# Kernel tuning notes

Hardware: AMD Instinct MI355X
Metric: run time of the kernel (lower is better)

## Reference

```python
import jax, jax.numpy as jnp
import numpy as np

NUM_HEADS = 8

def _gelu(x):
    return jax.nn.gelu(x, approximate=False)

def _ln(x, w, b, eps=1e-5):
    m = x.mean(-1, keepdims=True)
    v = ((x - m) ** 2).mean(-1, keepdims=True)
    return (x - m) / jnp.sqrt(v + eps) * w + b

def _conv(x, w, pad):
    return jax.lax.conv_general_dilated(x, w, (1, 1), [(pad, pad), (pad, pad)],
                                        dimension_numbers=('NCHW', 'OIHW', 'NCHW'))

def _dwconv(x, w):
    return jax.lax.conv_general_dilated(x, w, (1, 1), [(1, 1), (1, 1)],
                                        feature_group_count=x.shape[1],
                                        dimension_numbers=('NCHW', 'OIHW', 'NCHW'))

def setup_inputs():
    B, T, N, C, K = 4, 3, 4096, 256, 100
    ks = jax.random.split(jax.random.key(0), 16)
    p = lambda i, shape: (0.02 * jax.random.normal(ks[i], shape)).astype(jnp.float32)
    z = lambda n: jnp.zeros((n,), jnp.float32)
    return {
        'x': jax.random.normal(ks[0], (B, N, C), jnp.float32),
        'mem': jax.random.normal(ks[1], (B * T, N, C), jnp.float32),
        'conv1_w': p(2, (C, C, 7, 7)), 'conv1_b': z(C),
        'conv2_w': p(3, (C, C, 1, 1)), 'conv2_b': z(C),
        'conv3_w': p(4, (K, C, 1, 1)),
        'sim_alpha': jnp.ones((1,), jnp.float32), 'sim_beta': jnp.zeros((1,), jnp.float32),
        'ln_w': jnp.ones((C,), jnp.float32), 'ln_b': z(C),
        'q_w': p(5, (C, C)), 'q_b': z(C),
        'k_w': p(6, (C, C)), 'k_b': z(C),
        'v_w': p(7, (C, C)), 'v_b': z(C),
        'proj_w': p(8, (C, C)), 'proj_b': z(C),
        'fc1_w': p(9, (4 * C, C)), 'fc1_b': z(4 * C),
        'dw_w': p(10, (4 * C, 1, 3, 3)), 'dw_b': z(4 * C),
        'fc2_w': p(11, (C, 4 * C)), 'fc2_b': z(C),
        'H': 64, 'W': 64, 't': 3,
    }

def reference(x, mem, conv1_w, conv1_b, conv2_w, conv2_b, conv3_w, sim_alpha, sim_beta,
              ln_w, ln_b, q_w, q_b, k_w, k_b, v_w, v_b, proj_w, proj_b,
              fc1_w, fc1_b, dw_w, dw_b, fc2_w, fc2_b, H, W, t):
    B, N, C = x.shape
    T = t + 1
    # stack memory frames with current frame: [B, T, N, C]
    xt = jnp.concatenate([mem.reshape(B, t, N, C), x[:, None]], axis=1)
    img = xt.reshape(B * T, N, C).transpose(0, 2, 1).reshape(B * T, C, H, W)
    h = _gelu(_conv(img, conv1_w, 3) + conv1_b[:, None, None])
    h = _gelu(_conv(h, conv2_w, 0) + conv2_b[:, None, None])
    cz = _conv(h, conv3_w, 0)                      # [B*T, K, H, W]
    K = cz.shape[1]
    center = jax.nn.softmax(cz.reshape(B, T, K, N), axis=-1)
    center = jnp.einsum('btkn,btnc->btkc', center, xt)  # cluster centers [B,T,K,C]
    last, prev = center[:, -1], center[:, :-1]
    num = jnp.einsum('bkc,bskc->bsk', last, prev)
    den = jnp.maximum(jnp.linalg.norm(last, axis=-1)[:, None] * jnp.linalg.norm(prev, axis=-1), 1e-8)
    cos = jax.nn.sigmoid(sim_beta + sim_alpha * (num / den))  # [B, T-1, K]
    C_in = last + (cos[..., None] * prev).sum(axis=1)
    C_in = _ln(C_in, ln_w, ln_b)
    # cross-attention: queries = current frame tokens, keys/values = centers
    hd = C // NUM_HEADS
    q = (x @ q_w.T + q_b).reshape(B, N, NUM_HEADS, hd) * (hd ** -0.5)
    k = (C_in @ k_w.T + k_b).reshape(B, K, NUM_HEADS, hd)
    v = (C_in @ v_w.T + v_b).reshape(B, K, NUM_HEADS, hd)
    attn = jax.nn.softmax(jnp.einsum('bnhd,bkhd->bhnk', q, k), axis=-1)
    o = jnp.einsum('bhnk,bkhd->bnhd', attn, v).reshape(B, N, C)
    o = o @ proj_w.T + proj_b
    out = x + _ln(o, ln_w, ln_b)
    # MLP with depthwise conv
    y = out @ fc1_w.T + fc1_b                      # [B, N, 4C]
    yi = y.transpose(0, 2, 1).reshape(B, 4 * C, H, W)
    yi = _dwconv(yi, dw_w) + dw_b[:, None, None]
    y = _gelu(yi.reshape(B, 4 * C, N).transpose(0, 2, 1))
    y = y @ fc2_w.T + fc2_b
    return out + _ln(y, ln_w, ln_b)
```

## Files before the change

kernel.cpp:

```cpp
#include <hip/hip_runtime.h>
#include <math.h>

#define NN 4096
#define CC 256
#define HH 64
#define BT 16
#define KCC 100
#define NHH 8
#define HDD 32
#define C4 1024

typedef unsigned short bf16_t;
typedef short s16x8 __attribute__((ext_vector_type(8)));
typedef float f32x4 __attribute__((ext_vector_type(4)));
typedef float f32x16 __attribute__((ext_vector_type(16)));

__device__ __forceinline__ float bf2f(bf16_t h) {
  return __uint_as_float(((unsigned)h) << 16);
}
__device__ __forceinline__ bf16_t f2bf(float f) {
  unsigned u = __float_as_uint(f);
  return (bf16_t)((u + 0x7FFFu + ((u >> 16) & 1u)) >> 16);
}

__device__ __forceinline__ float gelu_f(float x) {
  return 0.5f * x * (1.0f + erff(x * 0.7071067811865475f));
}

__device__ __forceinline__ void g2l16(const void* g, void* l) {
  __builtin_amdgcn_global_load_lds((const __attribute__((address_space(1))) void*)g,
                                   (__attribute__((address_space(3))) void*)l, 16, 0, 0);
}

__device__ __forceinline__ float block_sum256(float v) {
  __shared__ float sh[4];
#pragma unroll
  for (int off = 32; off; off >>= 1) v += __shfl_xor(v, off, 64);
  __syncthreads();
  if ((threadIdx.x & 63) == 0) sh[threadIdx.x >> 6] = v;
  __syncthreads();
  return sh[0] + sh[1] + sh[2] + sh[3];
}

__device__ __forceinline__ const float* xt_base(const float* x, const float* mem, int bt) {
  int b = bt >> 2, tt = bt & 3;
  return (tt < 3) ? (mem + (size_t)(b * 3 + tt) * NN * CC)
                  : (x + (size_t)b * NN * CC);
}

__global__ __launch_bounds__(256) void prologue(const float* __restrict__ x,
                                                const float* __restrict__ mem,
                                                bf16_t* __restrict__ xtb,
                                                const float* __restrict__ w1,
                                                bf16_t* __restrict__ wtb,
                                                const float* __restrict__ c2w,
                                                const float* __restrict__ c3w,
                                                const float* __restrict__ qw,
                                                const float* __restrict__ pw,
                                                const float* __restrict__ f1w,
                                                const float* __restrict__ f2w,
                                                bf16_t* __restrict__ wbz) {
  int bid = blockIdx.x;
  int tid = threadIdx.x;
  if (bid < 16384) {
    int i = bid * 256 + tid;
    int c4 = i & 63;
    int n = (i >> 6) & 4095;
    int bt = i >> 18;
    const float* src = xt_base(x, mem, bt) + (size_t)n * CC + c4 * 4;
    float4 v = *(const float4*)src;
    ushort4 o;
    o.x = f2bf(v.x); o.y = f2bf(v.y); o.z = f2bf(v.z); o.w = f2bf(v.w);
    *(ushort4*)(xtb + (size_t)i * 4) = o;
  } else if (bid < 19520) {
    int i = (bid - 16384) * 256 + tid;
    int cj = i & 7;
    int t = i >> 3;
    int co = t & 63; t >>= 6;
    int oc = t & 3; t >>= 2;
    int kx = t % 7; t /= 7;
    int cq = t & 3; t >>= 2;
    int cg = t & 7;
    int ky = t >> 3;
    int ci = cg * 32 + oc * 8 + cj;
    int cog = cq * 64 + co;
    wtb[i] = f2bf(w1[((size_t)(cog * CC + ci) * 7 + ky) * 7 + kx]);
  } else {
    int j = (bid - 19520) * 256 + tid;
    float v;
    if (j < 65536) v = c2w[j];
    else if (j < 91136) v = c3w[j - 65536];
    else if (j < 156672) v = qw[j - 91136];
    else if (j < 222208) v = pw[j - 156672];
    else if (j < 484352) v = f1w[j - 222208];
    else v = f2w[j - 484352];
    wbz[j] = f2bf(v);
  }
}

__global__ __launch_bounds__(1024, 4) void conv1_mfma(const bf16_t* __restrict__ xtb,
                                                      const bf16_t* __restrict__ wtb,
                                                      const float* __restrict__ bias,
                                                      bf16_t* __restrict__ h1) {
  int bid = blockIdx.x;
  int cq = bid & 3;
  int rem = bid >> 2;
  int bt = rem & 15;
  int rb = rem >> 4;
  int r0 = rb * 16;
  int co0 = cq * 64;
  int tid = threadIdx.x;
  int wv = tid >> 6;
  int lane = tid & 63;
  int l31 = lane & 31;
  int h = lane >> 5;
  __shared__ __align__(16) short As[22][4][70][8];
  __shared__ __align__(16) short Ws[2][7][4][64][8];
  {
    s16x8 z = {0, 0, 0, 0, 0, 0, 0, 0};
    for (int i = tid; i < 22 * 4 * 70; i += 1024) *(s16x8*)((short*)As + i * 8) = z;
  }
  __syncthreads();
  f32x16 acc[2][2] = {};
  const bf16_t* xb = xtb + (size_t)bt * (NN * CC);
  for (int cig = 0; cig < 8; ++cig) {
    int ci0 = cig * 32;
    for (int t = wv; t < 88; t += 16) {
      int rr = t >> 2, go = t & 3;
      int r = r0 - 3 + rr;
      if (r >= 0 && r < HH) {
        const bf16_t* gsrc = xb + ((size_t)(r * 64 + lane)) * CC + ci0 + go * 8;
        g2l16(gsrc, &As[rr][go][3][0]);
      }
    }
    {
      const bf16_t* wk = wtb + ((size_t)((0 * 8 + cig) * 4 + cq)) * (1792 * 8);
      for (int t = wv; t < 28; t += 16)
        g2l16(wk + (size_t)t * 512 + lane * 8, (short*)Ws[0] + t * 512);
    }
    __syncthreads();
    for (int ky = 0; ky < 7; ++ky) {
      int cur = ky & 1;
      if (ky < 6) {
        const bf16_t* wk = wtb + ((size_t)(((ky + 1) * 8 + cig) * 4 + cq)) * (1792 * 8);
        for (int t = wv; t < 28; t += 16)
          g2l16(wk + (size_t)t * 512 + lane * 8, (short*)Ws[cur ^ 1] + t * 512);
      }
#pragma unroll
      for (int kx = 0; kx < 7; ++kx) {
        s16x8 fa[2][2], fb[2][2];
#pragma unroll
        for (int mt = 0; mt < 2; ++mt)
#pragma unroll
          for (int ks = 0; ks < 2; ++ks) {
            fa[mt][ks] = *(const s16x8*)&As[wv + ky][ks * 2 + h][mt * 32 + l31 + kx][0];
            fb[mt][ks] = *(const s16x8*)&Ws[cur][kx][ks * 2 + h][mt * 32 + l31][0];
          }
#pragma unroll
        for (int ks = 0; ks < 2; ++ks)
#pragma unroll
          for (int mt = 0; mt < 2; ++mt)
#pragma unroll
            for (int nt = 0; nt < 2; ++nt)
              acc[mt][nt] = __builtin_amdgcn_mfma_f32_32x32x16_bf16(
                  fa[mt][ks], fb[nt][ks], acc[mt][nt], 0, 0, 0);
      }
      __syncthreads();
    }
  }
  int row = r0 + wv;
  const size_t xbase = (size_t)bt * (NN * CC);
#pragma unroll
  for (int nt = 0; nt < 2; ++nt) {
    int co = co0 + nt * 32 + l31;
    float bs = bias[co];
#pragma unroll
    for (int mt = 0; mt < 2; ++mt) {
#pragma unroll
      for (int rg = 0; rg < 16; ++rg) {
        int px = mt * 32 + (rg & 3) + 8 * (rg >> 2) + 4 * h;
        float vv = acc[mt][nt][rg] + bs;
        h1[xbase + (size_t)(row * 64 + px) * CC + co] = f2bf(gelu_f(vv));
      }
    }
  }
}

__global__ __launch_bounds__(512) void conv23(const bf16_t* __restrict__ bh1,
                                              const bf16_t* __restrict__ w2,
                                              const float* __restrict__ b2,
                                              const bf16_t* __restrict__ w3,
                                              bf16_t* __restrict__ czt) {
  __shared__ __align__(16) char smem[126720];
  short (*As2)[72] = (short(*)[72])smem;
  short (*Bs2)[72] = (short(*)[72])(smem + 18432);
  short (*h2s)[264] = (short(*)[264])smem;
  short (*w3s)[264] = (short(*)[264])(smem + 67584);
  short (*ot)[132] = (short(*)[132])smem;
  int tid = threadIdx.x;
  int m0 = blockIdx.x * 128;
  int lane = tid & 63, wv = tid >> 6;
  int wm = wv & 1, wn = wv >> 1;
  int lm = lane & 15, g = lane >> 4;
  f32x4 acc[4][4] = {};
  int r1 = tid >> 2, kq = tid & 3;
  int br = tid >> 1, bq = (tid & 1) * 32;
  for (int k0 = 0; k0 < 256; k0 += 64) {
    *(s16x8*)&As2[r1][kq * 8] =
        *(const s16x8*)(bh1 + (size_t)(m0 + r1) * 256 + k0 + kq * 8);
    *(s16x8*)&As2[r1][32 + kq * 8] =
        *(const s16x8*)(bh1 + (size_t)(m0 + r1) * 256 + k0 + 32 + kq * 8);
#pragma unroll
    for (int j = 0; j < 4; ++j)
      *(s16x8*)&Bs2[br][bq + j * 8] =
          *(const s16x8*)(w2 + (size_t)br * 256 + k0 + bq + j * 8);
    __syncthreads();
#pragma unroll
    for (int ks = 0; ks < 2; ++ks) {
      s16x8 af[4], bf[4];
#pragma unroll
      for (int mt = 0; mt < 4; ++mt)
        af[mt] = *(const s16x8*)&As2[wm * 64 + mt * 16 + lm][ks * 32 + g * 8];
#pragma unroll
      for (int nt = 0; nt < 4; ++nt)
        bf[nt] = *(const s16x8*)&Bs2[wn * 64 + nt * 16 + lm][ks * 32 + g * 8];
#pragma unroll
      for (int mt = 0; mt < 4; ++mt)
#pragma unroll
        for (int nt = 0; nt < 4; ++nt)
          acc[mt][nt] = __builtin_amdgcn_mfma_f32_16x16x32_bf16(af[mt], bf[nt],
                                                                acc[mt][nt], 0, 0, 0);
    }
    __syncthreads();
  }
#pragma unroll
  for (int nt = 0; nt < 4; ++nt) {
    int c = wn * 64 + nt * 16 + lm;
    float bs = b2[c];
#pragma unroll
    for (int mt = 0; mt < 4; ++mt) {
#pragma unroll
      for (int rg = 0; rg < 4; ++rg) {
        int m = wm * 64 + mt * 16 + g * 4 + rg;
        h2s[m][c] = (short)f2bf(gelu_f(acc[mt][nt][rg] + bs));
      }
    }
  }
  {
    s16x8 z = {0, 0, 0, 0, 0, 0, 0, 0};
    for (int t = tid; t < 112 * 32; t += 512) {
      int rr = t >> 5, cc = (t & 31) * 8;
      s16x8 vv = z;
      if (rr < 100) vv = *(const s16x8*)(w3 + (size_t)rr * 256 + cc);
      *(s16x8*)&w3s[rr][cc] = vv;
    }
  }
  __syncthreads();
  f32x4 acc3[4][2] = {};
  int n_base = wn * 32;
#pragma unroll
  for (int k0 = 0; k0 < 256; k0 += 32) {
    s16x8 af[4], bf[2];
#pragma unroll
    for (int mt = 0; mt < 4; ++mt)
      af[mt] = *(const s16x8*)&h2s[wm * 64 + mt * 16 + lm][k0 + g * 8];
#pragma unroll
    for (int nt = 0; nt < 2; ++nt)
      bf[nt] = *(const s16x8*)&w3s[n_base + nt * 16 + lm][k0 + g * 8];
#pragma unroll
    for (int mt = 0; mt < 4; ++mt)
#pragma unroll
      for (int nt = 0; nt < 2; ++nt)
        acc3[mt][nt] = __builtin_amdgcn_mfma_f32_16x16x32_bf16(af[mt], bf[nt],
                                                               acc3[mt][nt], 0, 0, 0);
  }
  __syncthreads();
#pragma unroll
  for (int nt = 0; nt < 2; ++nt) {
    int kc = n_base + nt * 16 + lm;
    if (kc < 100) {
#pragma unroll
      for (int mt = 0; mt < 4; ++mt) {
#pragma unroll
        for (int rg = 0; rg < 4; ++rg) {
          int px = wm * 64 + mt * 16 + g * 4 + rg;
          ot[kc][px] = (short)f2bf(acc3[mt][nt][rg]);
        }
      }
    }
  }
  __syncthreads();
  for (int t = tid; t < 100 * 128; t += 512) {
    int kc = t >> 7, px = t & 127;
    czt[(size_t)kc * 65536 + m0 + px] = (bf16_t)ot[kc][px];
  }
}

template <int GELU, int BIAS, int TOUT, int OBF>
__global__ __launch_bounds__(256) void gemm_mfma(const bf16_t* __restrict__ A,
                                                 const bf16_t* __restrict__ W,
                                                 const float* __restrict__ bias,
                                                 void* __restrict__ outp,
                                                 int M, int N, int K, int ldo,
                                                 size_t aStr, size_t oStr) {
  __shared__ short As[128][72];
  __shared__ short Bs[128][72];
  A += (size_t)blockIdx.z * aStr;
  size_t obase = (size_t)blockIdx.z * oStr;
  int tid = threadIdx.x;
  int n0 = blockIdx.x * 128, m0 = blockIdx.y * 128;
  int lane = tid & 63, wv = tid >> 6;
  int wm = wv & 1, wn = wv >> 1;
  int lm = lane & 15, g = lane >> 4;
  f32x4 acc[4][4] = {};
  int r1 = tid >> 2, kq = tid & 3;
  int r2 = r1 + 64;
  for (int k0 = 0; k0 < K; k0 += 64) {
    *(s16x8*)&As[r1][kq * 8] = *(const s16x8*)(A + (size_t)(m0 + r1) * K + k0 + kq * 8);
    *(s16x8*)&As[r1][32 + kq * 8] =
        *(const s16x8*)(A + (size_t)(m0 + r1) * K + k0 + 32 + kq * 8);
    *(s16x8*)&As[r2][kq * 8] = *(const s16x8*)(A + (size_t)(m0 + r2) * K + k0 + kq * 8);
    *(s16x8*)&As[r2][32 + kq * 8] =
        *(const s16x8*)(A + (size_t)(m0 + r2) * K + k0 + 32 + kq * 8);
    s16x8 z = {0, 0, 0, 0, 0, 0, 0, 0};
    s16x8 b1 = z, b2 = z, b3 = z, b4 = z;
    if (n0 + r1 < N) {
      b1 = *(const s16x8*)(W + (size_t)(n0 + r1) * K + k0 + kq * 8);
      b2 = *(const s16x8*)(W + (size_t)(n0 + r1) * K + k0 + 32 + kq * 8);
    }
    if (n0 + r2 < N) {
      b3 = *(const s16x8*)(W + (size_t)(n0 + r2) * K + k0 + kq * 8);
      b4 = *(const s16x8*)(W + (size_t)(n0 + r2) * K + k0 + 32 + kq * 8);
    }
    *(s16x8*)&Bs[r1][kq * 8] = b1;
    *(s16x8*)&Bs[r1][32 + kq * 8] = b2;
    *(s16x8*)&Bs[r2][kq * 8] = b3;
    *(s16x8*)&Bs[r2][32 + kq * 8] = b4;
    __syncthreads();
#pragma unroll
    for (int ks = 0; ks < 2; ++ks) {
      s16x8 af[4], bf[4];
#pragma unroll
      for (int mt = 0; mt < 4; ++mt)
        af[mt] = *(const s16x8*)&As[wm * 64 + mt * 16 + lm][ks * 32 + g * 8];
#pragma unroll
      for (int nt = 0; nt < 4; ++nt)
        bf[nt] = *(const s16x8*)&Bs[wn * 64 + nt * 16 + lm][ks * 32 + g * 8];
#pragma unroll
      for (int mt = 0; mt < 4; ++mt)
#pragma unroll
        for (int nt = 0; nt < 4; ++nt)
          acc[mt][nt] = __builtin_amdgcn_mfma_f32_16x16x32_bf16(af[mt], bf[nt],
                                                                acc[mt][nt], 0, 0, 0);
    }
    __syncthreads();
  }
#pragma unroll
  for (int nt = 0; nt < 4; ++nt) {
    int n = n0 + wn * 64 + nt * 16 + lm;
    if (n >= N) continue;
    float bs = BIAS ? bias[n] : 0.f;
#pragma unroll
    for (int mt = 0; mt < 4; ++mt) {
#pragma unroll
      for (int rg = 0; rg < 4; ++rg) {
        int m = m0 + wm * 64 + mt * 16 + g * 4 + rg;
        float v = acc[mt][nt][rg] + bs;
        if (GELU) v = gelu_f(v);
        size_t idx = obase + (TOUT ? ((size_t)n * ldo + m) : ((size_t)m * ldo + n));
        if (OBF)
          ((bf16_t*)outp)[idx] = f2bf(v);
        else
          ((float*)outp)[idx] = v;
      }
    }
  }
}

__global__ __launch_bounds__(256) void gemm_kv(const float* __restrict__ cin,
                                               const float* __restrict__ kw,
                                               const float* __restrict__ kbias,
                                               const float* __restrict__ vw,
                                               const float* __restrict__ vbias,
                                               float* __restrict__ kout,
                                               float* __restrict__ vout) {
  const float* Wm = blockIdx.z ? vw : kw;
  const float* bias = blockIdx.z ? vbias : kbias;
  float* outp = blockIdx.z ? vout : kout;
  const int M = 400, N = 256, K = 256;
  __shared__ float As[16][68];
  __shared__ float Ws[16][68];
  int tid = threadIdx.x;
  int n0 = blockIdx.x * 64, m0 = blockIdx.y * 64;
  int txn = tid & 15, tym = tid >> 4;
  int mi = tid >> 2, kq = (tid & 3) * 4;
  float acc[4][4] = {};
  for (int k0 = 0; k0 < K; k0 += 16) {
    float4 av = {0, 0, 0, 0}, wvv = {0, 0, 0, 0};
    if (m0 + mi < M) av = *(const float4*)&cin[(size_t)(m0 + mi) * K + k0 + kq];
    if (n0 + mi < N) wvv = *(const float4*)&Wm[(size_t)(n0 + mi) * K + k0 + kq];
    As[kq + 0][mi] = av.x; As[kq + 1][mi] = av.y; As[kq + 2][mi] = av.z; As[kq + 3][mi] = av.w;
    Ws[kq + 0][mi] = wvv.x; Ws[kq + 1][mi] = wvv.y; Ws[kq + 2][mi] = wvv.z; Ws[kq + 3][mi] = wvv.w;
    __syncthreads();
#pragma unroll
    for (int ki = 0; ki < 16; ++ki) {
      float4 a4 = *(const float4*)&As[ki][tym * 4];
      float4 w4 = *(const float4*)&Ws[ki][txn * 4];
      float am[4] = {a4.x, a4.y, a4.z, a4.w};
      float wn[4] = {w4.x, w4.y, w4.z, w4.w};
#pragma unroll
      for (int i = 0; i < 4; ++i)
#pragma unroll
        for (int j = 0; j < 4; ++j) acc[i][j] += am[i] * wn[j];
    }
    __syncthreads();
  }
#pragma unroll
  for (int i = 0; i < 4; ++i) {
    int m = m0 + tym * 4 + i;
    if (m >= M) continue;
#pragma unroll
    for (int j = 0; j < 4; ++j) {
      int n = n0 + txn * 4 + j;
      outp[(size_t)m * 256 + n] = acc[i][j] + bias[n];
    }
  }
}

__global__ __launch_bounds__(256) void softmax_rows(bf16_t* __restrict__ p) {
  __shared__ float sh[8];
  int tid = threadIdx.x;
  bf16_t* base = p + (size_t)blockIdx.x * NN + tid * 16;
  s16x8 a = *(const s16x8*)base;
  s16x8 b = *(const s16x8*)(base + 8);
  float vals[16];
#pragma unroll
  for (int j = 0; j < 8; ++j) {
    vals[j] = bf2f((bf16_t)a[j]);
    vals[8 + j] = bf2f((bf16_t)b[j]);
  }
  float mx = -1e30f;
#pragma unroll
  for (int j = 0; j < 16; ++j) mx = fmaxf(mx, vals[j]);
#pragma unroll
  for (int off = 32; off; off >>= 1) mx = fmaxf(mx, __shfl_xor(mx, off, 64));
  if ((tid & 63) == 0) sh[tid >> 6] = mx;
  __syncthreads();
  mx = fmaxf(fmaxf(sh[0], sh[1]), fmaxf(sh[2], sh[3]));
  float s = 0.f;
#pragma unroll
  for (int j = 0; j < 16; ++j) {
    vals[j] = expf(vals[j] - mx);
    s += vals[j];
  }
#pragma unroll
  for (int off = 32; off; off >>= 1) s += __shfl_xor(s, off, 64);
  if ((tid & 63) == 0) sh[4 + (tid >> 6)] = s;
  __syncthreads();
  s = sh[4] + sh[5] + sh[6] + sh[7];
  float inv = 1.f / s;
  s16x8 oa, ob;
#pragma unroll
  for (int j = 0; j < 8; ++j) {
    oa[j] = (short)f2bf(vals[j] * inv);
    ob[j] = (short)f2bf(vals[8 + j] * inv);
  }
  *(s16x8*)base = oa;
  *(s16x8*)(base + 8) = ob;
}

__global__ __launch_bounds__(256) void center_mfma(const bf16_t* __restrict__ soft,
                                                   const bf16_t* __restrict__ xtb,
                                                   float* __restrict__ partial) {
  int c0 = blockIdx.x * 128;
  int bt = blockIdx.y;
  int nc = blockIdx.z;
  int tid = threadIdx.x;
  int lane = tid & 63, wv = tid >> 6;
  int wm = wv & 1, wn = wv >> 1;
  int lm = lane & 15, g = lane >> 4;
  __shared__ short As[128][40];
  __shared__ short Bs[128][40];
  f32x4 acc[4][4] = {};
  int r1 = tid >> 2, kq = tid & 3;
  int r2 = r1 + 64;
  int bk = tid & 31, bc = (tid >> 5) * 16;
  const bf16_t* sb = soft + (size_t)bt * NN + (size_t)nc * 512;
  const bf16_t* xb = xtb + ((size_t)bt * NN + (size_t)nc * 512) * CC + c0;
  for (int k0 = 0; k0 < 512; k0 += 32) {
    *(s16x8*)&As[r1][kq * 8] =
        *(const s16x8*)(sb + (size_t)r1 * (BT * NN) + k0 + kq * 8);
    if (r2 < KCC)
      *(s16x8*)&As[r2][kq * 8] =
          *(const s16x8*)(sb + (size_t)r2 * (BT * NN) + k0 + kq * 8);
    s16x8 v0 = *(const s16x8*)(xb + (size_t)(k0 + bk) * CC + bc);
    s16x8 v1 = *(const s16x8*)(xb + (size_t)(k0 + bk) * CC + bc + 8);
#pragma unroll
    for (int j = 0; j < 8; ++j) Bs[bc + j][bk] = v0[j];
#pragma unroll
    for (int j = 0; j < 8; ++j) Bs[bc + 8 + j][bk] = v1[j];
    __syncthreads();
    s16x8 af[4], bf[4];
#pragma unroll
    for (int mt = 0; mt < 4; ++mt)
      af[mt] = *(const s16x8*)&As[wm * 64 + mt * 16 + lm][g * 8];
#pragma unroll
    for (int nt = 0; nt < 4; ++nt)
      bf[nt] = *(const s16x8*)&Bs[wn * 64 + nt * 16 + lm][g * 8];
#pragma unroll
    for (int mt = 0; mt < 4; ++mt)
#pragma unroll
      for (int nt = 0; nt < 4; ++nt)
        acc[mt][nt] = __builtin_amdgcn_mfma_f32_16x16x32_bf16(af[mt], bf[nt],
                                                              acc[mt][nt], 0, 0, 0);
    __syncthreads();
  }
  size_t obase = ((size_t)nc * BT + bt) * (KCC * CC);
#pragma unroll
  for (int nt = 0; nt < 4; ++nt) {
    int c = c0 + wn * 64 + nt * 16 + lm;
#pragma unroll
    for (int mt = 0; mt < 4; ++mt) {
#pragma unroll
      for (int rg = 0; rg < 4; ++rg) {
        int m = wm * 64 + mt * 16 + g * 4 + rg;
        if (m < KCC) partial[obase + (size_t)m * CC + c] = acc[mt][nt][rg];
      }
    }
  }
}

__global__ __launch_bounds__(256) void sim_cin(const float* __restrict__ partial,
                                               const float* __restrict__ alpha_p,
                                               const float* __restrict__ beta_p,
                                               const float* __restrict__ lnw,
                                               const float* __restrict__ lnb,
                                               float* __restrict__ cin) {
  int b = blockIdx.x / KCC, kc = blockIdx.x % KCC;
  int c = threadIdx.x;
  float p0 = 0.f, p1 = 0.f, p2 = 0.f, lst = 0.f;
#pragma unroll
  for (int nc = 0; nc < 8; ++nc) {
    size_t base = ((size_t)nc * BT) * KCC * CC;
    p0 += partial[base + ((size_t)(b * 4 + 0) * KCC + kc) * CC + c];
    p1 += partial[base + ((size_t)(b * 4 + 1) * KCC + kc) * CC + c];
    p2 += partial[base + ((size_t)(b * 4 + 2) * KCC + kc) * CC + c];
    lst += partial[base + ((size_t)(b * 4 + 3) * KCC + kc) * CC + c];
  }
  float v7[7] = {lst * lst, p0 * p0, p1 * p1, p2 * p2,
                 lst * p0, lst * p1, lst * p2};
#pragma unroll
  for (int off = 32; off; off >>= 1)
#pragma unroll
    for (int j = 0; j < 7; ++j) v7[j] += __shfl_xor(v7[j], off, 64);
  __shared__ float sh7[4][8];
  if ((threadIdx.x & 63) == 0)
#pragma unroll
    for (int j = 0; j < 7; ++j) sh7[threadIdx.x >> 6][j] = v7[j];
  __syncthreads();
  float s7[7];
#pragma unroll
  for (int j = 0; j < 7; ++j)
    s7[j] = sh7[0][j] + sh7[1][j] + sh7[2][j] + sh7[3][j];
  float ll = s7[0], q0 = s7[1], q1 = s7[2], q2 = s7[3];
  float d0 = s7[4], d1 = s7[5], d2 = s7[6];
  float alpha = alpha_p[0], beta = beta_p[0];
  float nl = sqrtf(ll);
  float c0 = 1.f / (1.f + expf(-(beta + alpha * (d0 / fmaxf(nl * sqrtf(q0), 1e-8f)))));
  float c1 = 1.f / (1.f + expf(-(beta + alpha * (d1 / fmaxf(nl * sqrtf(q1), 1e-8f)))));
  float c2 = 1.f / (1.f + expf(-(beta + alpha * (d2 / fmaxf(nl * sqrtf(q2), 1e-8f)))));
  float v = lst + c0 * p0 + c1 * p1 + c2 * p2;
  float m = block_sum256(v) * (1.f / CC);
  float dv = v - m;
  float var = block_sum256(dv * dv) * (1.f / CC);
  cin[((size_t)b * KCC + kc) * CC + c] = dv * rsqrtf(var + 1e-5f) * lnw[c] + lnb[c];
}

__global__ __launch_bounds__(256) void attn2(const float* __restrict__ q,
                                             const float* __restrict__ kb,
                                             const float* __restrict__ vb,
                                             bf16_t* __restrict__ ob) {
  int b = blockIdx.y;
  int n0 = blockIdx.x * 8;
  int tid = threadIdx.x;
  __shared__ float qs[8][256];
  __shared__ float Ks[32][257];
  __shared__ float sc[8][8][104];
#pragma unroll
  for (int r = 0; r < 8; ++r)
    qs[r][tid] = q[((size_t)b * NN + n0 + r) * CC + tid] * 0.17677669529663687f;
  int nn = tid >> 5, kcl = tid & 31;
  for (int kt = 0; kt < 4; ++kt) {
    int kbase = kt * 32;
    int rows = (kbase + 32 <= KCC) ? 32 : (KCC - kbase);
    __syncthreads();
    for (int idx = tid; idx < rows * 256; idx += 256) {
      int rr = idx >> 8, cc = idx & 255;
      Ks[rr][cc] = kb[((size_t)b * KCC + kbase + rr) * CC + cc];
    }
    __syncthreads();
    if (kcl < rows) {
#pragma unroll
      for (int h = 0; h < NHH; ++h) {
        float s = 0.f;
#pragma unroll
        for (int d = 0; d < HDD; ++d) s += qs[nn][h * HDD + d] * Ks[kcl][h * HDD + d];
        sc[nn][h][kbase + kcl] = s;
      }
    }
  }
  __syncthreads();
  {
    int tnn = tid >> 5, th = (tid >> 2) & 7, j = tid & 3;
    float mx = -1e30f;
    for (int kc = j * 25; kc < j * 25 + 25; ++kc) mx = fmaxf(mx, sc[tnn][th][kc]);
    mx = fmaxf(mx, __shfl_xor(mx, 1, 64));
    mx = fmaxf(mx, __shfl_xor(mx, 2, 64));
    float sm = 0.f;
    for (int kc = j * 25; kc < j * 25 + 25; ++kc) {
      float e = expf(sc[tnn][th][kc] - mx);
      sc[tnn][th][kc] = e;
      sm += e;
    }
    sm += __shfl_xor(sm, 1, 64);
    sm += __shfl_xor(sm, 2, 64);
    float inv = 1.f / sm;
    for (int kc = j * 25; kc < j * 25 + 25; ++kc) sc[tnn][th][kc] *= inv;
  }
  __syncthreads();
  float o[8] = {0, 0, 0, 0, 0, 0, 0, 0};
  int h = tid >> 5;
  for (int kc = 0; kc < KCC; ++kc) {
    float v = vb[((size_t)b * KCC + kc) * CC + tid];
#pragma unroll
    for (int r = 0; r < 8; ++r) o[r] += sc[r][h][kc] * v;
  }
#pragma unroll
  for (int r = 0; r < 8; ++r)
    ob[((size_t)b * NN + n0 + r) * CC + tid] = f2bf(o[r]);
}

template <int WB>
__global__ __launch_bounds__(256) void add_ln(const float* __restrict__ res,
                                              const float* __restrict__ y,
                                              const float* __restrict__ lnw,
                                              const float* __restrict__ lnb,
                                              float* __restrict__ dst,
                                              bf16_t* __restrict__ dst_b) {
  size_t row = (size_t)blockIdx.x * 4 + (threadIdx.x >> 6);
  int lane = threadIdx.x & 63;
  int c = lane * 4;
  float4 v = *(const float4*)&y[row * CC + c];
  float s = v.x + v.y + v.z + v.w;
#pragma unroll
  for (int off = 32; off; off >>= 1) s += __shfl_xor(s, off, 64);
  float m = s * (1.f / CC);
  float d0 = v.x - m, d1 = v.y - m, d2 = v.z - m, d3 = v.w - m;
  float q = d0 * d0 + d1 * d1 + d2 * d2 + d3 * d3;
#pragma unroll
  for (int off = 32; off; off >>= 1) q += __shfl_xor(q, off, 64);
  float inv = rsqrtf(q * (1.f / CC) + 1e-5f);
  float4 r4 = *(const float4*)&res[row * CC + c];
  float4 lw = *(const float4*)&lnw[c];
  float4 lb = *(const float4*)&lnb[c];
  float4 o;
  o.x = r4.x + d0 * inv * lw.x + lb.x;
  o.y = r4.y + d1 * inv * lw.y + lb.y;
  o.z = r4.z + d2 * inv * lw.z + lb.z;
  o.w = r4.w + d3 * inv * lw.w + lb.w;
  *(float4*)&dst[row * CC + c] = o;
  if (WB) {
    ushort4 ob;
    ob.x = f2bf(o.x); ob.y = f2bf(o.y); ob.z = f2bf(o.z); ob.w = f2bf(o.w);
    *(ushort4*)&dst_b[row * CC + c] = ob;
  }
}

__global__ __launch_bounds__(256) void dwconv_kernel(const bf16_t* __restrict__ y1,
                                                     const float* __restrict__ dww,
                                                     const float* __restrict__ dwb,
                                                     bf16_t* __restrict__ y2) {
  int b = blockIdx.x >> 12;
  int n = blockIdx.x & 4095;
  int h = n >> 6, w = n & 63;
  int c40 = threadIdx.x * 4;
  float wreg[4][9];
#pragma unroll
  for (int j = 0; j < 4; ++j)
#pragma unroll
    for (int t2 = 0; t2 < 9; ++t2) wreg[j][t2] = dww[(size_t)(c40 + j) * 9 + t2];
  float acc[4] = {0, 0, 0, 0};
#pragma unroll
  for (int dy = 0; dy < 3; ++dy) {
    int r = h + dy - 1;
    if (r < 0 || r >= HH) continue;
#pragma unroll
    for (int dx = 0; dx < 3; ++dx) {
      int cl = w + dx - 1;
      if (cl < 0 || cl >= 64) continue;
      ushort4 u = *(const ushort4*)(y1 + ((size_t)b * NN + r * 64 + cl) * C4 + c40);
      int t2 = dy * 3 + dx;
      acc[0] += bf2f(u.x) * wreg[0][t2];
      acc[1] += bf2f(u.y) * wreg[1][t2];
      acc[2] += bf2f(u.z) * wreg[2][t2];
      acc[3] += bf2f(u.w) * wreg[3][t2];
    }
  }
  ushort4 o;
  o.x = f2bf(gelu_f(acc[0] + dwb[c40 + 0]));
  o.y = f2bf(gelu_f(acc[1] + dwb[c40 + 1]));
  o.z = f2bf(gelu_f(acc[2] + dwb[c40 + 2]));
  o.w = f2bf(gelu_f(acc[3] + dwb[c40 + 3]));
  *(ushort4*)(y2 + ((size_t)b * NN + n) * C4 + c40) = o;
}

extern "C" void kernel_launch(void* const* d_in, const int* in_sizes, int n_in,
                              void* d_out, int out_size, void* d_ws, size_t ws_size,
                              hipStream_t stream) {
  const float* x = (const float*)d_in[0];
  const float* mem = (const float*)d_in[1];
  const float* conv1_w = (const float*)d_in[2];
  const float* conv1_b = (const float*)d_in[3];
  const float* conv2_w = (const float*)d_in[4];
  const float* conv2_b = (const float*)d_in[5];
  const float* conv3_w = (const float*)d_in[6];
  const float* sim_a = (const float*)d_in[7];
  const float* sim_b = (const float*)d_in[8];
  const float* ln_w = (const float*)d_in[9];
  const float* ln_b = (const float*)d_in[10];
  const float* q_w = (const float*)d_in[11];
  const float* q_b = (const float*)d_in[12];
  const float* k_w = (const float*)d_in[13];
  const float* k_b = (const float*)d_in[14];
  const float* v_w = (const float*)d_in[15];
  const float* v_b = (const float*)d_in[16];
  const float* proj_w = (const float*)d_in[17];
  const float* proj_b = (const float*)d_in[18];
  const float* fc1_w = (const float*)d_in[19];
  const float* fc1_b = (const float*)d_in[20];
  const float* dw_w = (const float*)d_in[21];
  const float* dw_b = (const float*)d_in[22];
  const float* fc2_w = (const float*)d_in[23];
  const float* fc2_b = (const float*)d_in[24];

  char* base = (char*)d_ws;
  bf16_t* xtb = (bf16_t*)(base);
  bf16_t* by1 = (bf16_t*)(base);
  bf16_t* bh1 = (bf16_t*)(base + 33554432);
  float* qb = (float*)(base + 33554432);
  float* outb = (float*)(base + 33554432);
  float* partial = (float*)(base + 50331648);
  float* pbuf = (float*)(base + 50331648);
  bf16_t* y2 = (bf16_t*)(base + 50331648);
  bf16_t* czt = (bf16_t*)(base + 67108864);
  bf16_t* obz = (bf16_t*)(base + 67108864);
  bf16_t* outb_b = (bf16_t*)(base + 67108864);
  bf16_t* wtb = (bf16_t*)(base + 80216064);
  bf16_t* wbz = (bf16_t*)(base + 96993280);
  float* cin = (float*)(base + 100124672);
  float* kb = (float*)(base + 100534272);
  float* vb = (float*)(base + 100943872);
  float* dout = (float*)d_out;

  bf16_t* conv2_wb = wbz;
  bf16_t* conv3_wb = wbz + 65536;
  bf16_t* q_wb = wbz + 91136;
  bf16_t* proj_wb = wbz + 156672;
  bf16_t* fc1_wb = wbz + 222208;
  bf16_t* fc2_wb = wbz + 484352;

  prologue<<<22436, 256, 0, stream>>>(x, mem, xtb, conv1_w, wtb, conv2_w, conv3_w,
                                      q_w, proj_w, fc1_w, fc2_w, wbz);
  conv1_mfma<<<256, 1024, 0, stream>>>(xtb, wtb, conv1_b, bh1);
  conv23<<<512, 512, 0, stream>>>(bh1, conv2_wb, conv2_b, conv3_wb, czt);
  softmax_rows<<<1600, 256, 0, stream>>>(czt);
  center_mfma<<<dim3(2, 16, 8), 256, 0, stream>>>(czt, xtb, partial);
  sim_cin<<<400, 256, 0, stream>>>(partial, sim_a, sim_b, ln_w, ln_b, cin);
  gemm_mfma<0, 1, 0, 0><<<dim3(2, 32, 4), 256, 0, stream>>>(
      xtb + (size_t)3 * NN * CC, q_wb, q_b, qb, 4096, 256, 256, 256,
      (size_t)4 * NN * CC, (size_t)NN * CC);
  gemm_kv<<<dim3(4, 7, 2), 256, 0, stream>>>(cin, k_w, k_b, v_w, v_b, kb, vb);
  attn2<<<dim3(512, 4), 256, 0, stream>>>(qb, kb, vb, obz);
  gemm_mfma<0, 1, 0, 0><<<dim3(2, 128, 1), 256, 0, stream>>>(obz, proj_wb, proj_b, pbuf,
                                                             16384, 256, 256, 256, 0, 0);
  add_ln<1><<<4096, 256, 0, stream>>>(x, pbuf, ln_w, ln_b, outb, outb_b);
  gemm_mfma<0, 1, 0, 1><<<dim3(8, 128, 1), 256, 0, stream>>>(outb_b, fc1_wb, fc1_b, by1,
                                                             16384, 1024, 256, 1024, 0, 0);
  dwconv_kernel<<<16384, 256, 0, stream>>>(by1, dw_w, dw_b, y2);
  gemm_mfma<0, 1, 0, 0><<<dim3(2, 32, 4), 256, 0, stream>>>(
      y2, fc2_wb, fc2_b, dout, 4096, 256, 1024, 256,
      (size_t)NN * C4, (size_t)NN * CC);
  add_ln<0><<<4096, 256, 0, stream>>>(outb, dout, ln_w, ln_b, dout, nullptr);
}
```

Baseline: 804.8 us.

## Fuse proj/fc2 GEMMs with residual LayerNorm and add sliding-window dwconv

Adds a gemm_ln kernel where each block computes a full 128x256 output row tile with MFMA, stages it in shared memory and applies bias, LayerNorm and the residual add before storing. This replaces the separate proj and fc2 GEMMs plus two add_ln passes, removing the fp32 intermediate round trips through global memory. The depthwise conv now handles 16 consecutive pixels per block and keeps a sliding register window of columns, cutting redundant neighbour loads. The trade-off is fewer, larger blocks: 128 blocks for proj and 128 for fc2 at 512 threads with about 66KB of shared memory, which lowers parallelism.

```diff
diff --git a/kernel.cpp b/kernel.cpp
--- a/kernel.cpp
+++ b/kernel.cpp
@@ -377,6 +377,109 @@
   }
 }
 
+template <int WB>
+__global__ __launch_bounds__(512) void gemm_ln(const bf16_t* __restrict__ A,
+                                               const bf16_t* __restrict__ W,
+                                               const float* __restrict__ bias,
+                                               const float* __restrict__ lnw,
+                                               const float* __restrict__ lnb,
+                                               const float* __restrict__ res,
+                                               float* __restrict__ dst,
+                                               bf16_t* __restrict__ dst_b,
+                                               int K, size_t aStr, size_t oStr) {
+  __shared__ __align__(16) char smem[66560];
+  short (*As)[72] = (short(*)[72])smem;
+  short (*Bs)[72] = (short(*)[72])(smem + 18432);
+  float (*Ls)[260] = (float(*)[260])smem;
+  int tid = threadIdx.x;
+  int m0 = blockIdx.x * 128;
+  A += (size_t)blockIdx.y * aStr;
+  size_t obase = (size_t)blockIdx.y * oStr;
+  int lane = tid & 63, wv = tid >> 6;
+  int wm = wv & 1, wn = wv >> 1;
+  int lm = lane & 15, g = lane >> 4;
+  f32x4 acc[4][4] = {};
+  int r1 = tid >> 2, kq = tid & 3;
+  int br = tid >> 1, bq = (tid & 1) * 32;
+  for (int k0 = 0; k0 < K; k0 += 64) {
+    *(s16x8*)&As[r1][kq * 8] = *(const s16x8*)(A + (size_t)(m0 + r1) * K + k0 + kq * 8);
+    *(s16x8*)&As[r1][32 + kq * 8] =
+        *(const s16x8*)(A + (size_t)(m0 + r1) * K + k0 + 32 + kq * 8);
+#pragma unroll
+    for (int j = 0; j < 4; ++j)
+      *(s16x8*)&Bs[br][bq + j * 8] =
+          *(const s16x8*)(W + (size_t)br * K + k0 + bq + j * 8);
+    __syncthreads();
+#pragma unroll
+    for (int ks = 0; ks < 2; ++ks) {
+      s16x8 af[4], bf[4];
+#pragma unroll
+      for (int mt = 0; mt < 4; ++mt)
+        af[mt] = *(const s16x8*)&As[wm * 64 + mt * 16 + lm][ks * 32 + g * 8];
+#pragma unroll
+      for (int nt = 0; nt < 4; ++nt)
+        bf[nt] = *(const s16x8*)&Bs[wn * 64 + nt * 16 + lm][ks * 32 + g * 8];
+#pragma unroll
+      for (int mt = 0; mt < 4; ++mt)
+#pragma unroll
+        for (int nt = 0; nt < 4; ++nt)
+          acc[mt][nt] = __builtin_amdgcn_mfma_f32_16x16x32_bf16(af[mt], bf[nt],
+                                                                acc[mt][nt], 0, 0, 0);
+    }
+    __syncthreads();
+  }
+#pragma unroll
+  for (int ph = 0; ph < 2; ++ph) {
+    if (ph) __syncthreads();
+    if (wm == ph) {
+#pragma unroll
+      for (int nt = 0; nt < 4; ++nt) {
+        int c = wn * 64 + nt * 16 + lm;
+        float bs = bias[c];
+#pragma unroll
+        for (int mt = 0; mt < 4; ++mt) {
+#pragma unroll
+          for (int rg = 0; rg < 4; ++rg) {
+            int m = mt * 16 + g * 4 + rg;
+            Ls[m][c] = acc[mt][nt][rg] + bs;
+          }
+        }
+      }
+    }
+    __syncthreads();
+#pragma unroll
+    for (int i = 0; i < 8; ++i) {
+      int mr = wv * 8 + i;
+      size_t grow = (size_t)(m0 + ph * 64 + mr);
+      int c = lane * 4;
+      float4 v = *(const float4*)&Ls[mr][c];
+      float s = v.x + v.y + v.z + v.w;
+#pragma unroll
+      for (int off = 32; off; off >>= 1) s += __shfl_xor(s, off, 64);
+      float mmean = s * (1.f / CC);
+      float d0 = v.x - mmean, d1 = v.y - mmean, d2 = v.z - mmean, d3 = v.w - mmean;
+      float q = d0 * d0 + d1 * d1 + d2 * d2 + d3 * d3;
+#pragma unroll
+      for (int off = 32; off; off >>= 1) q += __shfl_xor(q, off, 64);
+      float inv = rsqrtf(q * (1.f / CC) + 1e-5f);
+      float4 r4 = *(const float4*)&res[obase + grow * CC + c];
+      float4 lw = *(const float4*)&lnw[c];
+      float4 lb = *(const float4*)&lnb[c];
+      float4 o;
+      o.x = r4.x + d0 * inv * lw.x + lb.x;
+      o.y = r4.y + d1 * inv * lw.y + lb.y;
+      o.z = r4.z + d2 * inv * lw.z + lb.z;
+      o.w = r4.w + d3 * inv * lw.w + lb.w;
+      *(float4*)&dst[obase + grow * CC + c] = o;
+      if (WB) {
+        ushort4 ob;
+        ob.x = f2bf(o.x); ob.y = f2bf(o.y); ob.z = f2bf(o.z); ob.w = f2bf(o.w);
+        *(ushort4*)&dst_b[obase + grow * CC + c] = ob;
+      }
+    }
+  }
+}
+
 __global__ __launch_bounds__(256) void gemm_kv(const float* __restrict__ cin,
                                                const float* __restrict__ kw,
                                                const float* __restrict__ kbias,
@@ -640,78 +743,70 @@
     ob[((size_t)b * NN + n0 + r) * CC + tid] = f2bf(o[r]);
 }
 
-template <int WB>
-__global__ __launch_bounds__(256) void add_ln(const float* __restrict__ res,
-                                              const float* __restrict__ y,
-                                              const float* __restrict__ lnw,
-                                              const float* __restrict__ lnb,
-                                              float* __restrict__ dst,
-                                              bf16_t* __restrict__ dst_b) {
-  size_t row = (size_t)blockIdx.x * 4 + (threadIdx.x >> 6);
-  int lane = threadIdx.x & 63;
-  int c = lane * 4;
-  float4 v = *(const float4*)&y[row * CC + c];
-  float s = v.x + v.y + v.z + v.w;
-#pragma unroll
-  for (int off = 32; off; off >>= 1) s += __shfl_xor(s, off, 64);
-  float m = s * (1.f / CC);
-  float d0 = v.x - m, d1 = v.y - m, d2 = v.z - m, d3 = v.w - m;
-  float q = d0 * d0 + d1 * d1 + d2 * d2 + d3 * d3;
-#pragma unroll
-  for (int off = 32; off; off >>= 1) q += __shfl_xor(q, off, 64);
-  float inv = rsqrtf(q * (1.f / CC) + 1e-5f);
-  float4 r4 = *(const float4*)&res[row * CC + c];
-  float4 lw = *(const float4*)&lnw[c];
-  float4 lb = *(const float4*)&lnb[c];
-  float4 o;
-  o.x = r4.x + d0 * inv * lw.x + lb.x;
-  o.y = r4.y + d1 * inv * lw.y + lb.y;
-  o.z = r4.z + d2 * inv * lw.z + lb.z;
-  o.w = r4.w + d3 * inv * lw.w + lb.w;
-  *(float4*)&dst[row * CC + c] = o;
-  if (WB) {
-    ushort4 ob;
-    ob.x = f2bf(o.x); ob.y = f2bf(o.y); ob.z = f2bf(o.z); ob.w = f2bf(o.w);
-    *(ushort4*)&dst_b[row * CC + c] = ob;
-  }
-}
-
 __global__ __launch_bounds__(256) void dwconv_kernel(const bf16_t* __restrict__ y1,
                                                      const float* __restrict__ dww,
                                                      const float* __restrict__ dwb,
                                                      bf16_t* __restrict__ y2) {
-  int b = blockIdx.x >> 12;
-  int n = blockIdx.x & 4095;
-  int h = n >> 6, w = n & 63;
+  int t = blockIdx.x;
+  int b = t >> 8;
+  int h = (t >> 2) & 63;
+  int qd = t & 3;
+  int w0 = qd << 4;
   int c40 = threadIdx.x * 4;
   float wreg[4][9];
 #pragma unroll
   for (int j = 0; j < 4; ++j)
 #pragma unroll
-    for (int t2 = 0; t2 < 9; ++t2) wreg[j][t2] = dww[(size_t)(c40 + j) * 9 + t2];
-  float acc[4] = {0, 0, 0, 0};
+    for (int k = 0; k < 9; ++k) wreg[j][k] = dww[(size_t)(c40 + j) * 9 + k];
+  float b4[4];
+#pragma unroll
+  for (int j = 0; j < 4; ++j) b4[j] = dwb[c40 + j];
+  const bf16_t* bb = y1 + (size_t)b * NN * C4 + c40;
+  bf16_t* obp = y2 + (size_t)b * NN * C4 + c40;
+  ushort4 z4; z4.x = 0; z4.y = 0; z4.z = 0; z4.w = 0;
+  bool rok[3];
+  size_t rbase[3];
 #pragma unroll
   for (int dy = 0; dy < 3; ++dy) {
-    int r = h + dy - 1;
-    if (r < 0 || r >= HH) continue;
-#pragma unroll
-    for (int dx = 0; dx < 3; ++dx) {
-      int cl = w + dx - 1;
-      if (cl < 0 || cl >= 64) continue;
-      ushort4 u = *(const ushort4*)(y1 + ((size_t)b * NN + r * 64 + cl) * C4 + c40);
-      int t2 = dy * 3 + dx;
-      acc[0] += bf2f(u.x) * wreg[0][t2];
-      acc[1] += bf2f(u.y) * wreg[1][t2];
-      acc[2] += bf2f(u.z) * wreg[2][t2];
-      acc[3] += bf2f(u.w) * wreg[3][t2];
-    }
-  }
-  ushort4 o;
-  o.x = f2bf(gelu_f(acc[0] + dwb[c40 + 0]));
-  o.y = f2bf(gelu_f(acc[1] + dwb[c40 + 1]));
-  o.z = f2bf(gelu_f(acc[2] + dwb[c40 + 2]));
-  o.w = f2bf(gelu_f(acc[3] + dwb[c40 + 3]));
-  *(ushort4*)(y2 + ((size_t)b * NN + n) * C4 + c40) = o;
+    int r = h - 1 + dy;
+    rok[dy] = (r >= 0 && r < HH);
+    rbase[dy] = (size_t)(rok[dy] ? r : 0) * 64 * C4;
+  }
+  ushort4 u0[3], u1[3], u2[3];
+#pragma unroll
+  for (int dy = 0; dy < 3; ++dy) {
+    u0[dy] = (rok[dy] && w0 > 0) ? *(const ushort4*)(bb + rbase[dy] + (size_t)(w0 - 1) * C4) : z4;
+    u1[dy] = rok[dy] ? *(const ushort4*)(bb + rbase[dy] + (size_t)w0 * C4) : z4;
+  }
+  for (int w = w0; w < w0 + 16; ++w) {
+    bool cok = (w + 1 < 64);
+#pragma unroll
+    for (int dy = 0; dy < 3; ++dy)
+      u2[dy] = (rok[dy] && cok) ? *(const ushort4*)(bb + rbase[dy] + (size_t)(w + 1) * C4) : z4;
+    float acc0 = 0.f, acc1 = 0.f, acc2 = 0.f, acc3 = 0.f;
+#pragma unroll
+    for (int dy = 0; dy < 3; ++dy) {
+      acc0 += bf2f(u0[dy].x) * wreg[0][dy * 3 + 0] + bf2f(u1[dy].x) * wreg[0][dy * 3 + 1] +
+              bf2f(u2[dy].x) * wreg[0][dy * 3 + 2];
+      acc1 += bf2f(u0[dy].y) * wreg[1][dy * 3 + 0] + bf2f(u1[dy].y) * wreg[1][dy * 3 + 1] +
+              bf2f(u2[dy].y) * wreg[1][dy * 3 + 2];
+      acc2 += bf2f(u0[dy].z) * wreg[2][dy * 3 + 0] + bf2f(u1[dy].z) * wreg[2][dy * 3 + 1] +
+              bf2f(u2[dy].z) * wreg[2][dy * 3 + 2];
+      acc3 += bf2f(u0[dy].w) * wreg[3][dy * 3 + 0] + bf2f(u1[dy].w) * wreg[3][dy * 3 + 1] +
+              bf2f(u2[dy].w) * wreg[3][dy * 3 + 2];
+    }
+    ushort4 o;
+    o.x = f2bf(gelu_f(acc0 + b4[0]));
+    o.y = f2bf(gelu_f(acc1 + b4[1]));
+    o.z = f2bf(gelu_f(acc2 + b4[2]));
+    o.w = f2bf(gelu_f(acc3 + b4[3]));
+    *(ushort4*)(obp + (size_t)(h * 64 + w) * C4) = o;
+#pragma unroll
+    for (int dy = 0; dy < 3; ++dy) {
+      u0[dy] = u1[dy];
+      u1[dy] = u2[dy];
+    }
+  }
 }
 
 extern "C" void kernel_launch(void* const* d_in, const int* in_sizes, int n_in,
@@ -749,9 +844,8 @@
   bf16_t* bh1 = (bf16_t*)(base + 33554432);
   float* qb = (float*)(base + 33554432);
   float* outb = (float*)(base + 33554432);
+  bf16_t* y2 = (bf16_t*)(base + 50331648);
   float* partial = (float*)(base + 50331648);
-  float* pbuf = (float*)(base + 50331648);
-  bf16_t* y2 = (bf16_t*)(base + 50331648);
   bf16_t* czt = (bf16_t*)(base + 67108864);
   bf16_t* obz = (bf16_t*)(base + 67108864);
   bf16_t* outb_b = (bf16_t*)(base + 67108864);
@@ -781,14 +875,12 @@
       (size_t)4 * NN * CC, (size_t)NN * CC);
   gemm_kv<<<dim3(4, 7, 2), 256, 0, stream>>>(cin, k_w, k_b, v_w, v_b, kb, vb);
   attn2<<<dim3(512, 4), 256, 0, stream>>>(qb, kb, vb, obz);
-  gemm_mfma<0, 1, 0, 0><<<dim3(2, 128, 1), 256, 0, stream>>>(obz, proj_wb, proj_b, pbuf,
-                                                             16384, 256, 256, 256, 0, 0);
-  add_ln<1><<<4096, 256, 0, stream>>>(x, pbuf, ln_w, ln_b, outb, outb_b);
+  gemm_ln<1><<<dim3(128, 1), 512, 0, stream>>>(obz, proj_wb, proj_b, ln_w, ln_b,
+                                               x, outb, outb_b, 256, 0, 0);
   gemm_mfma<0, 1, 0, 1><<<dim3(8, 128, 1), 256, 0, stream>>>(outb_b, fc1_wb, fc1_b, by1,
                                                              16384, 1024, 256, 1024, 0, 0);
-  dwconv_kernel<<<16384, 256, 0, stream>>>(by1, dw_w, dw_b, y2);
-  gemm_mfma<0, 1, 0, 0><<<dim3(2, 32, 4), 256, 0, stream>>>(
-      y2, fc2_wb, fc2_b, dout, 4096, 256, 1024, 256,
-      (size_t)NN * C4, (size_t)NN * CC);
-  add_ln<0><<<4096, 256, 0, stream>>>(outb, dout, ln_w, ln_b, dout, nullptr);
-}
+  dwconv_kernel<<<1024, 256, 0, stream>>>(by1, dw_w, dw_b, y2);
+  gemm_ln<0><<<dim3(32, 4), 512, 0, stream>>>(y2, fc2_wb, fc2_b, ln_w, ln_b,
+                                              outb, dout, nullptr, 1024,
+                                              (size_t)NN * C4, (size_t)NN * CC);
+}
```

New measurement: 771.4 us (median of 2 runs). -4.1%, faster.
